# Optimization experiments

Hardware: AMD Instinct MI355X
Metric: run time of the kernel (lower is better)

The kernel has to match this reference:

```python
import jax, jax.numpy as jnp
from jax import lax
import numpy as np

B, N, D = 8, 4096, 64
S = 1024          # groups
K = 32            # kneighbors
RADIUS = 0.2


def farthest_point_sample(xyz, npoint):
    """xyz: [B,N,3] -> centroid indices [B,npoint]. Deterministic start at index 0
    (original torch uses a random start index)."""
    b, n, _ = xyz.shape

    def step(carry, _):
        distance, farthest = carry                              # [B,N], [B]
        centroid = jnp.take_along_axis(xyz, farthest[:, None, None], axis=1)  # [B,1,3]
        dist = jnp.sum((xyz - centroid) ** 2, axis=-1)          # [B,N]
        distance = jnp.minimum(distance, dist)
        new_far = jnp.argmax(distance, axis=-1)
        return (distance, new_far), farthest

    init = (jnp.full((b, n), 1e10, xyz.dtype), jnp.zeros((b,), jnp.int32))
    _, cents = lax.scan(step, init, None, length=npoint)        # [npoint,B]
    return cents.T                                              # [B,npoint]


def square_distance(src, dst):
    # [B,N,M] squared euclidean distances
    d = -2.0 * jnp.einsum('bnc,bmc->bnm', src, dst)
    d += jnp.sum(src ** 2, -1)[:, :, None]
    d += jnp.sum(dst ** 2, -1)[:, None, :]
    return d


def query_ball_point(radius, nsample, xyz, new_xyz):
    b, n, _ = xyz.shape
    s = new_xyz.shape[1]
    sqrdists = square_distance(new_xyz, xyz)                    # [B,S,N]
    arange = jnp.arange(n, dtype=jnp.int32)[None, None, :]
    group_idx = jnp.where(sqrdists > radius ** 2, n, arange)    # [B,S,N]
    group_idx = jnp.sort(group_idx, axis=-1)[:, :, :nsample]    # [B,S,K]
    first = group_idx[:, :, :1]
    group_idx = jnp.where(group_idx == n, first, group_idx)
    return group_idx


def gather_points(points, idx):
    # points [B,N,C], idx [B,...] -> [B,...,C]
    return jax.vmap(lambda p, i: p[i])(points, idx)


def setup_inputs() -> dict:
    key = jax.random.key(0)
    k1, k2 = jax.random.split(key)
    xyz = jax.random.uniform(k1, (B, N, 3), dtype=jnp.float32)
    points = jax.random.normal(k2, (B, N, D), dtype=jnp.float32)
    return {"xyz": xyz, "points": points}


def reference(xyz, points):
    fps_idx = farthest_point_sample(xyz, S)                     # [B,S]
    new_xyz = gather_points(xyz, fps_idx)                       # [B,S,3]
    anchor_feat = gather_points(points, fps_idx)                # [B,S,D]
    idx = query_ball_point(RADIUS, K, xyz, new_xyz)             # [B,S,K]
    grouped_xyz = gather_points(xyz, idx)                       # [B,S,K,3]
    grouped_points = gather_points(points, idx)                 # [B,S,K,D]
    grouped_points = jnp.concatenate([grouped_points, grouped_xyz], axis=-1)  # use_xyz
    anchor_rep = jnp.broadcast_to(anchor_feat[:, :, None, :], (B, S, K, D))
    new_points = jnp.concatenate([grouped_points, anchor_rep], axis=-1)  # [B,S,K,2D+3]
    return new_xyz, new_points
```

## Files before the change

### kernel.cpp

```cpp
#include <hip/hip_runtime.h>

#define BB 8
#define NN 4096
#define DD 64
#define SS 1024
#define KK 32
#define R2 0.04f

typedef float f32x2 __attribute__((ext_vector_type(2)));

#define DPP_MAXF(wv, CTRL)                                                             \
    {                                                                                  \
        int _o = __builtin_amdgcn_update_dpp(__float_as_int(wv), __float_as_int(wv),   \
                                             CTRL, 0xf, 0xf, false);                   \
        (wv) = fmaxf((wv), __int_as_float(_o));                                        \
    }

__global__ __launch_bounds__(512) void fused_kernel(const float* __restrict__ xyz,
                                                    const float* __restrict__ points,
                                                    float* __restrict__ out) {
#pragma clang fp contract(off)
    __shared__ float4 sxyz[NN];
    __shared__ unsigned long long red[SS];
    __shared__ int sfar[SS];
    __shared__ int bbuf[8][KK];
    __shared__ unsigned long long lpad[392];

    const int tid  = threadIdx.x;
    const int wave = tid >> 6;
    const int lane = tid & 63;
    const int b    = blockIdx.x >> 5;
    const int cs   = blockIdx.x & 31;
    const float* xb = xyz + (size_t)b * NN * 3;
    const float* pb = points + (size_t)b * NN * DD;

    for (int i = tid; i < SS; i += 512) red[i] = 0ull;
    for (int i = tid; i < 392; i += 512) lpad[i] = 0ull;

    {
        const float4* xb4 = (const float4*)(xb + tid * 24);
        const float4 q0 = xb4[0], q1 = xb4[1], q2 = xb4[2];
        const float4 q3 = xb4[3], q4 = xb4[4], q5 = xb4[5];
        float sx[8], sy[8], sz[8];
        sx[0] = q0.x; sy[0] = q0.y; sz[0] = q0.z;
        sx[1] = q0.w; sy[1] = q1.x; sz[1] = q1.y;
        sx[2] = q1.z; sy[2] = q1.w; sz[2] = q2.x;
        sx[3] = q2.y; sy[3] = q2.z; sz[3] = q2.w;
        sx[4] = q3.x; sy[4] = q3.y; sz[4] = q3.z;
        sx[5] = q3.w; sy[5] = q4.x; sz[5] = q4.y;
        sx[6] = q4.z; sy[6] = q4.w; sz[6] = q5.x;
        sx[7] = q5.y; sy[7] = q5.z; sz[7] = q5.w;
#pragma unroll
        for (int j = 0; j < 8; ++j)
            sxyz[tid * 8 + j] = make_float4(sx[j], sy[j], sz[j], 0.0f);
    }
    __syncthreads();

    const int tmax = cs * 32 + 32;

    if (tid < 256) {
        f32x2 px[8], py[8], pz[8], dist[8];
#pragma unroll
        for (int jj = 0; jj < 8; ++jj) {
            const float4 p0 = sxyz[tid * 16 + 2 * jj];
            const float4 p1 = sxyz[tid * 16 + 2 * jj + 1];
            px[jj] = (f32x2){p0.x, p1.x};
            py[jj] = (f32x2){p0.y, p1.y};
            pz[jj] = (f32x2){p0.z, p1.z};
            dist[jj] = (f32x2){1e10f, 1e10f};
        }
        int far = (int)(unsigned)lpad[0];

        for (int t = 0; t < tmax; ++t) {
            if (tid == 0) sfar[t] = far;
            const float4 c = sxyz[far];
            const f32x2 cx2 = (f32x2){c.x, c.x}, cy2 = (f32x2){c.y, c.y},
                        cz2 = (f32x2){c.z, c.z};

            f32x2 nd[8];
#pragma unroll
            for (int jj = 0; jj < 8; ++jj) {
                const f32x2 dx = px[jj] - cx2;
                const f32x2 dy = py[jj] - cy2;
                const f32x2 dz = pz[jj] - cz2;
                const f32x2 d  = (dx * dx + dy * dy) + dz * dz;
                f32x2 m;
                m.x = fminf(dist[jj].x, d.x);
                m.y = fminf(dist[jj].y, d.y);
                dist[jj] = m;
                nd[jj] = m;
            }
            const float m0 = fmaxf(fmaxf(nd[0].x, nd[0].y), nd[1].x);
            const float m1 = fmaxf(fmaxf(nd[1].y, nd[2].x), nd[2].y);
            const float m2 = fmaxf(fmaxf(nd[3].x, nd[3].y), nd[4].x);
            const float m3 = fmaxf(fmaxf(nd[4].y, nd[5].x), nd[5].y);
            const float m4 = fmaxf(fmaxf(nd[6].x, nd[6].y), nd[7].x);
            const float A  = fmaxf(fmaxf(m0, m1), m2);
            const float B  = fmaxf(fmaxf(m3, m4), nd[7].y);
            const float bestv = fmaxf(A, B);
            int localj = 0;
#pragma unroll
            for (int j = 15; j >= 0; --j) {
                const float v = (j & 1) ? nd[j >> 1].y : nd[j >> 1].x;
                if (v == bestv) localj = j;
            }

            float wv = bestv;
            DPP_MAXF(wv, 0x111);
            DPP_MAXF(wv, 0x112);
            DPP_MAXF(wv, 0x114);
            DPP_MAXF(wv, 0x118);
            DPP_MAXF(wv, 0x142);
            DPP_MAXF(wv, 0x143);
            const float maxw =
                __int_as_float(__builtin_amdgcn_readlane(__float_as_int(wv), 63));

            const unsigned long long hits = __ballot(bestv == maxw);
            const int L = __ffsll(hits) - 1;
            if (lane == L) {
                atomicMax(&red[t],
                          ((unsigned long long)__float_as_uint(bestv) << 32) |
                              (unsigned)~(unsigned)(tid * 16 + localj));
            }
            __syncthreads();
            far = (int)~(unsigned)red[t];
        }
    } else {
        for (int t = 0; t < tmax; ++t) __syncthreads();
    }

#pragma unroll
    for (int i = 0; i < 4; ++i) {
        const int s  = cs * 32 + wave * 4 + i;
        const int g  = b * SS + s;
        const int qi = sfar[s];
        const float4 q = sxyz[qi];
        const float qn = __fadd_rn(__fadd_rn(__fmul_rn(q.x, q.x), __fmul_rn(q.y, q.y)),
                                   __fmul_rn(q.z, q.z));

        int total = 0;
        for (int base = 0; base < NN && total < KK; base += 64) {
            const int n = base + lane;
            const float4 p = sxyz[n];
            const float pn = __fadd_rn(__fadd_rn(__fmul_rn(p.x, p.x), __fmul_rn(p.y, p.y)),
                                       __fmul_rn(p.z, p.z));
            const float dt = __fadd_rn(__fadd_rn(__fmul_rn(q.x, p.x), __fmul_rn(q.y, p.y)),
                                       __fmul_rn(q.z, p.z));
            const float d = __fadd_rn(__fadd_rn(__fmul_rn(-2.0f, dt), qn), pn);
            const bool hit = !(d > R2);
            const unsigned long long mask = __ballot(hit);
            const int before = __popcll(mask & ((1ull << lane) - 1ull));
            const int pos = total + before;
            if (hit && pos < KK) bbuf[wave][pos] = n;
            total += (int)__popcll(mask);
        }
        if (lane < KK) {
            const int v = (lane < total) ? bbuf[wave][lane] : bbuf[wave][0];
            bbuf[wave][lane] = v;
        }

        if (lane < 3)
            out[(size_t)g * 3 + lane] = (lane == 0) ? q.x : (lane == 1) ? q.y : q.z;

        const float a1 = (lane >= 3) ? pb[qi * DD + (lane - 3)] : 0.0f;
        const float a2 = (lane < 3) ? pb[qi * DD + (61 + lane)] : 0.0f;

        float* outp = out + (size_t)BB * SS * 3 + (size_t)g * (KK * 131);
        for (int k = 0; k < KK; ++k) {
            const int idx = bbuf[wave][k];
            const float4 pi = sxyz[idx];
            outp[k * 131 + lane] = pb[idx * DD + lane];
            const float v1 = (lane == 0) ? pi.x
                           : (lane == 1) ? pi.y
                           : (lane == 2) ? pi.z
                                         : a1;
            outp[k * 131 + 64 + lane] = v1;
            if (lane < 3) outp[k * 131 + 128 + lane] = a2;
        }
    }
}

extern "C" void kernel_launch(void* const* d_in, const int* in_sizes, int n_in,
                              void* d_out, int out_size, void* d_ws, size_t ws_size,
                              hipStream_t stream) {
    const float* xyz    = (const float*)d_in[0];
    const float* points = (const float*)d_in[1];
    float* out = (float*)d_out;

    fused_kernel<<<BB * 32, 512, 0, stream>>>(xyz, points, out);
}
```

Baseline: 853.8 us.

## Run FPS on two waves with spin-flag exchange instead of block barriers

The farthest-point-sampling loop now runs on 2 waves with 32 points per lane instead of 4 waves with 16 points per lane. The per-iteration __syncthreads plus shared atomicMax is replaced by a volatile double-buffered slot that each wave writes and then spins on for its peer's tagged value. The local argmax becomes a tree reduction that carries indices, and launch bounds now request 2 blocks per CU. This aims to cut barrier cost on the serial FPS chain, at the price of more registers per lane, longer per-lane work, and a spin-wait that relies on wave co-scheduling and volatile LDS ordering.

```diff
diff --git a/kernel.cpp b/kernel.cpp
--- a/kernel.cpp
+++ b/kernel.cpp
@@ -16,15 +16,15 @@
         (wv) = fmaxf((wv), __int_as_float(_o));                                        \
     }
 
-__global__ __launch_bounds__(512) void fused_kernel(const float* __restrict__ xyz,
-                                                    const float* __restrict__ points,
-                                                    float* __restrict__ out) {
+__global__ __launch_bounds__(512, 2) void fused_kernel(const float* __restrict__ xyz,
+                                                       const float* __restrict__ points,
+                                                       float* __restrict__ out) {
 #pragma clang fp contract(off)
     __shared__ float4 sxyz[NN];
-    __shared__ unsigned long long red[SS];
     __shared__ int sfar[SS];
     __shared__ int bbuf[8][KK];
-    __shared__ unsigned long long lpad[392];
+    volatile __shared__ unsigned long long slot[2][2];
+    __shared__ unsigned long long lpad[1408];
 
     const int tid  = threadIdx.x;
     const int wave = tid >> 6;
@@ -34,8 +34,10 @@
     const float* xb = xyz + (size_t)b * NN * 3;
     const float* pb = points + (size_t)b * NN * DD;
 
-    for (int i = tid; i < SS; i += 512) red[i] = 0ull;
-    for (int i = tid; i < 392; i += 512) lpad[i] = 0ull;
+    if (tid == 0) {
+        slot[0][0] = 0ull; slot[0][1] = 0ull; slot[1][0] = 0ull; slot[1][1] = 0ull;
+    }
+    for (int i = tid; i < 1408; i += 512) lpad[i] = 0ull;
 
     {
         const float4* xb4 = (const float4*)(xb + tid * 24);
@@ -58,16 +60,17 @@
 
     const int tmax = cs * 32 + 32;
 
-    if (tid < 256) {
-        f32x2 px[8], py[8], pz[8], dist[8];
-#pragma unroll
-        for (int jj = 0; jj < 8; ++jj) {
-            const float4 p0 = sxyz[tid * 16 + 2 * jj];
-            const float4 p1 = sxyz[tid * 16 + 2 * jj + 1];
-            px[jj] = (f32x2){p0.x, p1.x};
-            py[jj] = (f32x2){p0.y, p1.y};
-            pz[jj] = (f32x2){p0.z, p1.z};
-            dist[jj] = (f32x2){1e10f, 1e10f};
+    if (wave < 2) {
+        const int base = (wave << 11) + lane * 32;
+        f32x2 px[16], py[16], pz[16], dist[16];
+#pragma unroll
+        for (int u = 0; u < 16; ++u) {
+            const float4 p0 = sxyz[base + 2 * u];
+            const float4 p1 = sxyz[base + 2 * u + 1];
+            px[u] = (f32x2){p0.x, p1.x};
+            py[u] = (f32x2){p0.y, p1.y};
+            pz[u] = (f32x2){p0.z, p1.z};
+            dist[u] = (f32x2){1e10f, 1e10f};
         }
         int far = (int)(unsigned)lpad[0];
 
@@ -77,33 +80,43 @@
             const f32x2 cx2 = (f32x2){c.x, c.x}, cy2 = (f32x2){c.y, c.y},
                         cz2 = (f32x2){c.z, c.z};
 
-            f32x2 nd[8];
-#pragma unroll
-            for (int jj = 0; jj < 8; ++jj) {
-                const f32x2 dx = px[jj] - cx2;
-                const f32x2 dy = py[jj] - cy2;
-                const f32x2 dz = pz[jj] - cz2;
+#pragma unroll
+            for (int u = 0; u < 16; ++u) {
+                const f32x2 dx = px[u] - cx2;
+                const f32x2 dy = py[u] - cy2;
+                const f32x2 dz = pz[u] - cz2;
                 const f32x2 d  = (dx * dx + dy * dy) + dz * dz;
                 f32x2 m;
-                m.x = fminf(dist[jj].x, d.x);
-                m.y = fminf(dist[jj].y, d.y);
-                dist[jj] = m;
-                nd[jj] = m;
-            }
-            const float m0 = fmaxf(fmaxf(nd[0].x, nd[0].y), nd[1].x);
-            const float m1 = fmaxf(fmaxf(nd[1].y, nd[2].x), nd[2].y);
-            const float m2 = fmaxf(fmaxf(nd[3].x, nd[3].y), nd[4].x);
-            const float m3 = fmaxf(fmaxf(nd[4].y, nd[5].x), nd[5].y);
-            const float m4 = fmaxf(fmaxf(nd[6].x, nd[6].y), nd[7].x);
-            const float A  = fmaxf(fmaxf(m0, m1), m2);
-            const float B  = fmaxf(fmaxf(m3, m4), nd[7].y);
-            const float bestv = fmaxf(A, B);
-            int localj = 0;
-#pragma unroll
-            for (int j = 15; j >= 0; --j) {
-                const float v = (j & 1) ? nd[j >> 1].y : nd[j >> 1].x;
-                if (v == bestv) localj = j;
-            }
+                m.x = fminf(dist[u].x, d.x);
+                m.y = fminf(dist[u].y, d.y);
+                dist[u] = m;
+            }
+            float v1[16]; int g1[16];
+#pragma unroll
+            for (int u = 0; u < 16; ++u) {
+                v1[u] = fmaxf(dist[u].x, dist[u].y);
+                g1[u] = (dist[u].x == v1[u]) ? (2 * u) : (2 * u + 1);
+            }
+            float v2[8]; int g2[8];
+#pragma unroll
+            for (int u = 0; u < 8; ++u) {
+                v2[u] = fmaxf(v1[2 * u], v1[2 * u + 1]);
+                g2[u] = (v1[2 * u] == v2[u]) ? g1[2 * u] : g1[2 * u + 1];
+            }
+            float v3[4]; int g3[4];
+#pragma unroll
+            for (int u = 0; u < 4; ++u) {
+                v3[u] = fmaxf(v2[2 * u], v2[2 * u + 1]);
+                g3[u] = (v2[2 * u] == v3[u]) ? g2[2 * u] : g2[2 * u + 1];
+            }
+            float v4[2]; int g4[2];
+#pragma unroll
+            for (int u = 0; u < 2; ++u) {
+                v4[u] = fmaxf(v3[2 * u], v3[2 * u + 1]);
+                g4[u] = (v3[2 * u] == v4[u]) ? g3[2 * u] : g3[2 * u + 1];
+            }
+            const float bestv = fmaxf(v4[0], v4[1]);
+            const int bestg = base + ((v4[0] == bestv) ? g4[0] : g4[1]);
 
             float wv = bestv;
             DPP_MAXF(wv, 0x111);
@@ -114,20 +127,28 @@
             DPP_MAXF(wv, 0x143);
             const float maxw =
                 __int_as_float(__builtin_amdgcn_readlane(__float_as_int(wv), 63));
-
             const unsigned long long hits = __ballot(bestv == maxw);
             const int L = __ffsll(hits) - 1;
-            if (lane == L) {
-                atomicMax(&red[t],
-                          ((unsigned long long)__float_as_uint(bestv) << 32) |
-                              (unsigned)~(unsigned)(tid * 16 + localj));
-            }
-            __syncthreads();
-            far = (int)~(unsigned)red[t];
-        }
-    } else {
-        for (int t = 0; t < tmax; ++t) __syncthreads();
-    }
+            const int gW = __builtin_amdgcn_readlane(bestg, L);
+
+            const unsigned long long mine =
+                ((unsigned long long)(unsigned)(t + 1) << 52) |
+                ((unsigned long long)__float_as_uint(maxw) << 20) |
+                (unsigned long long)(unsigned)(4095 - gW);
+            if (lane == 0) slot[t & 1][wave] = mine;
+            unsigned long long peer;
+            do {
+                peer = slot[t & 1][1 - wave];
+            } while ((unsigned)(peer >> 52) != (unsigned)(t + 1));
+
+            const unsigned long long M52 = (1ull << 52) - 1ull;
+            unsigned long long best = mine & M52;
+            const unsigned long long pl = peer & M52;
+            if (pl > best) best = pl;
+            far = 4095 - (int)(best & 0xFFFull);
+        }
+    }
+    __syncthreads();
 
 #pragma unroll
     for (int i = 0; i < 4; ++i) {
@@ -139,8 +160,8 @@
                                    __fmul_rn(q.z, q.z));
 
         int total = 0;
-        for (int base = 0; base < NN && total < KK; base += 64) {
-            const int n = base + lane;
+        for (int base2 = 0; base2 < NN && total < KK; base2 += 64) {
+            const int n = base2 + lane;
             const float4 p = sxyz[n];
             const float pn = __fadd_rn(__fadd_rn(__fmul_rn(p.x, p.x), __fmul_rn(p.y, p.y)),
                                        __fmul_rn(p.z, p.z));
@@ -170,11 +191,11 @@
             const int idx = bbuf[wave][k];
             const float4 pi = sxyz[idx];
             outp[k * 131 + lane] = pb[idx * DD + lane];
-            const float v1 = (lane == 0) ? pi.x
-                           : (lane == 1) ? pi.y
-                           : (lane == 2) ? pi.z
-                                         : a1;
-            outp[k * 131 + 64 + lane] = v1;
+            const float v1c = (lane == 0) ? pi.x
+                            : (lane == 1) ? pi.y
+                            : (lane == 2) ? pi.z
+                                          : a1;
+            outp[k * 131 + 64 + lane] = v1c;
             if (lane < 3) outp[k * 131 + 128 + lane] = a2;
         }
     }
```

Measured after the change: 1.075 ms. +25.9%, slower.
